# Kernel optimization log

Measured on AMD Instinct MI355X. Metric: run time of the kernel, lower is better.

## Reference

```python
import jax, jax.numpy as jnp
import numpy as np

SEQ, B, N, H, OUT, K, L = 32, 1024, 19, 128, 1, 2, 2


def setup_inputs() -> dict:
    key = jax.random.key(0)
    ks = jax.random.split(key, 16)
    s = lambda i, shape, scale=1.0: (jax.random.normal(ks[i], shape, jnp.float32) * scale)
    return {
        "inputs": s(0, (SEQ, B, N, OUT)),
        "initial_hidden_state": s(1, (L, B, N * H)),
        "support": s(2, (N, N)) * (1.0 / np.sqrt(N)),
        "W_gate0": s(3, (3 * (OUT + H), 2 * H)) * 0.05,
        "b_gate0": s(4, (2 * H,)) * 0.05,
        "W_cand0": s(5, (3 * (OUT + H), H)) * 0.05,
        "b_cand0": s(6, (H,)) * 0.05,
        "W_gate1": s(7, (3 * (H + H), 2 * H)) * 0.05,
        "b_gate1": s(8, (2 * H,)) * 0.05,
        "W_cand1": s(9, (3 * (H + H), H)) * 0.05,
        "b_cand1": s(10, (H,)) * 0.05,
        "W_proj": s(11, (H, OUT)) * 0.05,
        "b_proj": s(12, (OUT,)) * 0.05,
    }


def reference(inputs, initial_hidden_state, support, W_gate0, b_gate0, W_cand0,
              b_cand0, W_gate1, b_gate1, W_cand1, b_cand1, W_proj, b_proj):
    seq_len, batch = inputs.shape[0], inputs.shape[1]
    h0 = initial_hidden_state.reshape(L, batch, N, H)

    def gconv(x, W, b):
        # Chebyshev diffusion: x0, T1=S@x0, T2=2*S@T1-x0 (K=2, 1 support)
        x0 = x
        x1 = jnp.einsum('mn,bnf->bmf', support, x0)
        feats = [x0, x1]
        for _ in range(K - 1):
            x2 = 2.0 * jnp.einsum('mn,bnf->bmf', support, x1) - x0
            feats.append(x2)
            x0, x1 = x1, x2
        X = jnp.concatenate(feats, axis=-1)  # (B, N, F*num_matrices)
        return jnp.einsum('bnf,fo->bno', X, W) + b

    def cell(x_in, h, Wg, bg, Wc, bc):
        ru = jax.nn.sigmoid(gconv(jnp.concatenate([x_in, h], axis=-1), Wg, bg))
        r, u = jnp.split(ru, 2, axis=-1)
        c = jnp.tanh(gconv(jnp.concatenate([x_in, r * h], axis=-1), Wc, bc))
        return u * h + (1.0 - u) * c

    layer_params = [(W_gate0, b_gate0, W_cand0, b_cand0),
                    (W_gate1, b_gate1, W_cand1, b_cand1)]

    def step(carry, _):
        h, cur = carry
        new_h = []
        x = cur
        for i, (Wg, bg, Wc, bc) in enumerate(layer_params):
            x = cell(x, h[i], Wg, bg, Wc, bc)
            new_h.append(x)
        proj = jnp.einsum('bnh,ho->bno', x, W_proj) + b_proj  # (B, N, OUT)
        out_t = proj.reshape(batch, N * OUT)
        return (jnp.stack(new_h, axis=0), proj), out_t

    go = jnp.zeros((batch, N, OUT), inputs.dtype)
    (_, _), outputs = jax.lax.scan(step, (h0, go), None, length=seq_len)
    return outputs  # (seq_len, batch, N*OUT)
```

## Files before the change

### kernel.cpp

```cpp
#include <hip/hip_runtime.h>
#include <hip/hip_bf16.h>
#include <math.h>

#define SEQ   32
#define BATCH 1024
#define NN    19
#define HH    128
#define NB    4
#define MR    (NB*NN)
#define SAS   264
#define H0S   128
#define H1S   132
#define UBS   128
#define NBLK  (BATCH/NB)
#define NT    512
#define UST_S 40

#define OFF_G0 0
#define OFF_C0 122880
#define OFF_G1 184320
#define OFF_C1 380928
#define WTOT   479232

#define OFF_H0  0
#define OFF_H1  19456
#define OFF_SA  59584
#define OFF_UB  101824
#define OFF_SBF 121280
#define OFF_UST 139712
#define OFF_XP  160192
#define LDS_BYTES 160496

__device__ unsigned short g_wall[WTOT];
__device__ unsigned short g_sbf[2*9*512];

typedef __attribute__((ext_vector_type(8))) short  bf16x8;
typedef __attribute__((ext_vector_type(4))) short  bf16x4;
typedef __attribute__((ext_vector_type(4))) float  f32x4;

__device__ __forceinline__ unsigned short f2bf(float v) {
    __hip_bfloat16 b = __float2bfloat16(v);
    return *reinterpret_cast<unsigned short*>(&b);
}
__device__ __forceinline__ float bf2f(unsigned short u) {
    unsigned int x = ((unsigned int)u) << 16;
    return __uint_as_float(x);
}
__device__ __forceinline__ float hload(const unsigned short* p) { return bf2f(*p); }
__device__ __forceinline__ float hload(const float* p)          { return *p; }
__device__ __forceinline__ void  hstore(unsigned short* p, float v) { *p = f2bf(v); }
__device__ __forceinline__ void  hstore(float* p, float v)          { *p = v; }

__global__ __launch_bounds__(256) void wconv_kernel(
    const float* __restrict__ W, int F, int O, int KP, int off, int l0)
{
    int idx = blockIdx.x*256 + threadIdx.x;
    int total = 3*O*KP;
    if (idx >= total) return;
    int j   = idx / (O*KP);
    int r   = idx - j*(O*KP);
    int col = r / KP;
    int k   = r - col*KP;
    int src;
    if (l0) src = (k < HH) ? k+1 : ((k == HH) ? 0 : -1);
    else    src = (k < F) ? k : -1;
    float v = (src >= 0) ? W[(size_t)(j*F + src)*O + col] : 0.f;
    g_wall[off + idx] = f2bf(v);
}

__global__ __launch_bounds__(256) void sbf_kernel(const float* __restrict__ S)
{
    __shared__ float sS[NN*NN], sS2[NN*NN];
    int tid = threadIdx.x;
    for (int i = tid; i < NN*NN; i += 256) sS[i] = S[i];
    __syncthreads();
    for (int i = tid; i < NN*NN; i += 256) {
        int m = i/NN, n = i - m*NN;
        float a = 0.f;
        for (int k = 0; k < NN; ++k) a += sS[m*NN+k]*sS[k*NN+n];
        sS2[i] = a;
    }
    __syncthreads();
    const int fmt[9] = {0,1,2, 1,2,3,4, 3,4};
    const int fkt[9] = {0,0,0, 1,1,1,1, 2,2};
    for (int idx = tid; idx < 2*9*512; idx += 256) {
        int mat = idx / 4608;
        int rem = idx - mat*4608;
        int i   = rem >> 9;
        int l   = (rem >> 3) & 63;
        int e   = rem & 7;
        int r   = fmt[i]*16 + (l & 15);
        int k   = fkt[i]*32 + (l >> 4)*8 + e;
        float v = 0.f;
        if (r < MR) {
            int b = r / NN, m = r - b*NN;
            int k0 = b*NN;
            if (k >= k0 && k < k0 + NN) {
                int n = k - k0;
                v = (mat == 0) ? sS[m*NN+n]
                               : (2.f*sS2[m*NN+n] - ((m==n)?1.f:0.f));
            }
        }
        g_sbf[idx] = f2bf(v);
    }
}

template<int KS, int NTC, bool GATE, int XW, typename HT, int HSTR>
__device__ __forceinline__ void gconv_phase(
    const unsigned short* __restrict__ BT, const float* __restrict__ bias,
    HT* __restrict__ hL,
    unsigned short* __restrict__ sA, unsigned short* __restrict__ ub,
    const unsigned short* __restrict__ sbf, unsigned short* __restrict__ Ust,
    int lane, int w)
{
    constexpr int OC = NTC*128;
    constexpr int KP = KS*32;
    const int r16 = lane & 15, quad = lane >> 4;
    const int sgo = w*(NTC*16);

    const unsigned short* wb[3][NTC];
    #pragma unroll
    for (int j = 0; j < 3; ++j)
        #pragma unroll
        for (int nt = 0; nt < NTC; ++nt)
            wb[j][nt] = BT + (size_t)(j*OC + sgo + nt*16 + r16)*KP + quad*8;

    f32x4 acc[3][5][NTC];
    #pragma unroll
    for (int j = 0; j < 3; ++j)
        #pragma unroll
        for (int mt = 0; mt < 5; ++mt)
            #pragma unroll
            for (int nt = 0; nt < NTC; ++nt) acc[j][mt][nt] = (f32x4)0.f;

    bf16x8 ring[2][3][NTC];
    #pragma unroll
    for (int j = 0; j < 3; ++j)
        #pragma unroll
        for (int nt = 0; nt < NTC; ++nt) {
            ring[0][j][nt] = *(const bf16x8*)(wb[j][nt]);
            if (KS > 1) ring[1][j][nt] = *(const bf16x8*)(wb[j][nt] + 32);
        }
    #pragma unroll
    for (int ks = 0; ks < KS; ++ks) {
        bf16x8 bcur[3][NTC];
        #pragma unroll
        for (int j = 0; j < 3; ++j)
            #pragma unroll
            for (int nt = 0; nt < NTC; ++nt) bcur[j][nt] = ring[ks & 1][j][nt];
        if (ks + 2 < KS) {
            #pragma unroll
            for (int j = 0; j < 3; ++j)
                #pragma unroll
                for (int nt = 0; nt < NTC; ++nt)
                    ring[ks & 1][j][nt] =
                        *(const bf16x8*)(wb[j][nt] + (ks + 2)*32);
        }
        #pragma unroll
        for (int mt = 0; mt < 5; ++mt) {
            bf16x8 af = *(const bf16x8*)&sA[(mt*16 + r16)*SAS + ks*32 + quad*8];
            #pragma unroll
            for (int j = 0; j < 3; ++j)
                #pragma unroll
                for (int nt = 0; nt < NTC; ++nt)
                    acc[j][mt][nt] = __builtin_amdgcn_mfma_f32_16x16x32_bf16(
                        af, bcur[j][nt], acc[j][mt][nt], 0, 0, 0);
        }
    }

    constexpr int ktCnt[3]   = {3,4,2};
    constexpr int ktMT[3][4] = {{0,1,2,0},{1,2,3,4},{3,4,0,0}};
    constexpr int ktF0[3]    = {0,3,7};
    #pragma unroll
    for (int j = 1; j <= 2; ++j) {
        #pragma unroll
        for (int kt = 0; kt < 3; ++kt) {
            if (kt == 2) {
                int zc = lane & 31, zh = lane >> 5;
                *(bf16x8*)&Ust[zc*UST_S + 16 + zh*8] = (bf16x8)(short)0;
            }
            #pragma unroll
            for (int mtk = 0; mtk < 2; ++mtk) {
                constexpr int dummy = 0; (void)dummy;
                int mt = kt*2 + mtk;
                if (kt*2 + mtk < 5) {
                    #pragma unroll
                    for (int nt = 0; nt < NTC; ++nt) {
                        bf16x4 pv;
                        pv[0] = (short)f2bf(acc[j][kt*2+mtk][nt][0]);
                        pv[1] = (short)f2bf(acc[j][kt*2+mtk][nt][1]);
                        pv[2] = (short)f2bf(acc[j][kt*2+mtk][nt][2]);
                        pv[3] = (short)f2bf(acc[j][kt*2+mtk][nt][3]);
                        *(bf16x4*)&Ust[(nt*16 + r16)*UST_S + mtk*16 + quad*4] = pv;
                    }
                }
                (void)mt;
            }
            bf16x8 Bf[NTC];
            #pragma unroll
            for (int nt = 0; nt < NTC; ++nt)
                Bf[nt] = *(const bf16x8*)&Ust[(nt*16 + r16)*UST_S + quad*8];
            #pragma unroll
            for (int q = 0; q < ktCnt[kt]; ++q) {
                const int mt = ktMT[kt][q];
                bf16x8 af = *(const bf16x8*)
                    &sbf[((j-1)*9 + ktF0[kt] + q)*512 + lane*8];
                #pragma unroll
                for (int nt = 0; nt < NTC; ++nt)
                    acc[0][mt][nt] = __builtin_amdgcn_mfma_f32_16x16x32_bf16(
                        af, Bf[nt], acc[0][mt][nt], 0, 0, 0);
            }
        }
    }

    float bv[NTC];
    #pragma unroll
    for (int nt = 0; nt < NTC; ++nt) bv[nt] = bias[sgo + nt*16 + r16];

    if (GATE) __syncthreads();

    #pragma unroll
    for (int mt = 0; mt < 5; ++mt)
        #pragma unroll
        for (int reg = 0; reg < 4; ++reg) {
            int gm = mt*16 + quad*4 + reg;
            if (gm < MR) {
                #pragma unroll
                for (int nt = 0; nt < NTC; ++nt) {
                    int o = sgo + nt*16 + r16;
                    float v = acc[0][mt][nt][reg] + bv[nt];
                    if (GATE) {
                        float sg_ = 1.f/(1.f + __expf(-v));
                        if (o < HH)
                            sA[gm*SAS + XW + o] =
                                f2bf(sg_ * hload(&hL[gm*HSTR + o]));
                        else
                            ub[gm*UBS + (o - HH)] = f2bf(sg_);
                    } else {
                        float c  = 2.f/(1.f + __expf(-2.f*v)) - 1.f;
                        float u  = bf2f(ub[gm*UBS + o]);
                        float ho = hload(&hL[gm*HSTR + o]);
                        hstore(&hL[gm*HSTR + o], u*ho + (1.f - u)*c);
                    }
                }
            }
        }
}

__global__ __launch_bounds__(NT, 2) void dcgru_persistent(
    const float* __restrict__ ihs,
    const float* __restrict__ bg0, const float* __restrict__ bc0,
    const float* __restrict__ bg1, const float* __restrict__ bc1,
    const float* __restrict__ Wp, const float* __restrict__ bp,
    float* __restrict__ out)
{
    extern __shared__ char smem[];
    unsigned short* h0  = (unsigned short*)(smem + OFF_H0);
    float*          h1  = (float*)(smem + OFF_H1);
    unsigned short* sA  = (unsigned short*)(smem + OFF_SA);
    unsigned short* ub  = (unsigned short*)(smem + OFF_UB);
    unsigned short* sbf = (unsigned short*)(smem + OFF_SBF);
    float*       xprev  = (float*)(smem + OFF_XP);

    const int tid  = threadIdx.x;
    const int lane = tid & 63;
    const int w    = tid >> 6;
    const int bb   = blockIdx.x * NB;
    unsigned short* Ust = (unsigned short*)(smem + OFF_UST) + w*(32*UST_S);

    const unsigned short* BTg0 = g_wall + OFF_G0;
    const unsigned short* BTc0 = g_wall + OFF_C0;
    const unsigned short* BTg1 = g_wall + OFF_G1;
    const unsigned short* BTc1 = g_wall + OFF_C1;

    for (int i = tid; i < MR*HH; i += NT) {
        h0[i] = f2bf(ihs[(size_t)bb*2432 + i]);
        h1[(i >> 7)*H1S + (i & 127)] = ihs[(size_t)(BATCH + bb)*2432 + i];
    }
    for (int i = tid; i < MR; i += NT) xprev[i] = 0.f;
    for (int i = tid; i < 80*SAS/8; i += NT) ((bf16x8*)sA)[i] = (bf16x8)(short)0;
    for (int i = tid; i < 2*9*512/8; i += NT)
        ((bf16x8*)sbf)[i] = ((const bf16x8*)g_sbf)[i];
    const float wp0 = Wp[lane], wp1 = Wp[64 + lane], bpv = bp[0];
    __syncthreads();

    for (int t = 0; t < SEQ; ++t) {
        for (int i = tid; i < MR*16; i += NT) {
            int row = i >> 4, ch = i & 15;
            *(bf16x8*)&sA[row*SAS + ch*8] =
                *(const bf16x8*)&h0[row*H0S + ch*8];
        }
        for (int i = tid; i < MR*4; i += NT) {
            int row = i >> 2, ch = i & 3;
            bf16x8 v = (bf16x8)(short)0;
            if (ch == 0) v[0] = (short)f2bf(xprev[row]);
            *(bf16x8*)&sA[row*SAS + HH + ch*8] = v;
        }
        __syncthreads();
        gconv_phase<5,2,true ,0,unsigned short,H0S>(BTg0, bg0, h0, sA, ub, sbf, Ust, lane, w);
        __syncthreads();
        gconv_phase<5,1,false,0,unsigned short,H0S>(BTc0, bc0, h0, sA, ub, sbf, Ust, lane, w);
        __syncthreads();

        for (int i = tid; i < MR*16; i += NT) {
            int row = i >> 4, ch = i & 15;
            *(bf16x8*)&sA[row*SAS + ch*8] =
                *(const bf16x8*)&h0[row*H0S + ch*8];
        }
        for (int i = tid; i < MR*16; i += NT) {
            int row = i >> 4, ch = i & 15;
            const float* hp = &h1[row*H1S + ch*8];
            f32x4 x0 = *(const f32x4*)hp;
            f32x4 x1 = *(const f32x4*)(hp + 4);
            bf16x8 v;
            v[0] = (short)f2bf(x0[0]); v[1] = (short)f2bf(x0[1]);
            v[2] = (short)f2bf(x0[2]); v[3] = (short)f2bf(x0[3]);
            v[4] = (short)f2bf(x1[0]); v[5] = (short)f2bf(x1[1]);
            v[6] = (short)f2bf(x1[2]); v[7] = (short)f2bf(x1[3]);
            *(bf16x8*)&sA[row*SAS + HH + ch*8] = v;
        }
        __syncthreads();
        gconv_phase<8,2,true ,HH,float,H1S>(BTg1, bg1, h1, sA, ub, sbf, Ust, lane, w);
        __syncthreads();
        gconv_phase<8,1,false,HH,float,H1S>(BTc1, bc1, h1, sA, ub, sbf, Ust, lane, w);
        __syncthreads();

        {
            int b  = w >> 1;
            int n0 = (w & 1) ? 10 : 0;
            int n1 = (w & 1) ? 19 : 10;
            for (int n = n0; n < n1; ++n) {
                int row = b*NN + n;
                float s = h1[row*H1S + lane]*wp0 + h1[row*H1S + 64 + lane]*wp1;
                #pragma unroll
                for (int off = 32; off; off >>= 1) s += __shfl_down(s, off, 64);
                if (lane == 0) {
                    float v = s + bpv;
                    out[((size_t)t*BATCH + bb + b)*NN + n] = v;
                    xprev[row] = v;
                }
            }
        }
        __syncthreads();
    }
}

extern "C" void kernel_launch(void* const* d_in, const int* in_sizes, int n_in,
                              void* d_out, int out_size, void* d_ws, size_t ws_size,
                              hipStream_t stream) {
    const float* ihs = (const float*)d_in[1];
    const float* S   = (const float*)d_in[2];
    const float* Wg0 = (const float*)d_in[3];
    const float* bg0 = (const float*)d_in[4];
    const float* Wc0 = (const float*)d_in[5];
    const float* bc0 = (const float*)d_in[6];
    const float* Wg1 = (const float*)d_in[7];
    const float* bg1 = (const float*)d_in[8];
    const float* Wc1 = (const float*)d_in[9];
    const float* bc1 = (const float*)d_in[10];
    const float* Wp  = (const float*)d_in[11];
    const float* bp  = (const float*)d_in[12];
    float* out = (float*)d_out;

    sbf_kernel<<<1, 256, 0, stream>>>(S);
    wconv_kernel<<<(3*256*160+255)/256, 256, 0, stream>>>(Wg0, 129, 256, 160, OFF_G0, 1);
    wconv_kernel<<<(3*128*160+255)/256, 256, 0, stream>>>(Wc0, 129, 128, 160, OFF_C0, 1);
    wconv_kernel<<<(3*256*256+255)/256, 256, 0, stream>>>(Wg1, 256, 256, 256, OFF_G1, 0);
    wconv_kernel<<<(3*128*256+255)/256, 256, 0, stream>>>(Wc1, 256, 128, 256, OFF_C1, 0);

    hipFuncSetAttribute((const void*)dcgru_persistent,
                        hipFuncAttributeMaxDynamicSharedMemorySize, LDS_BYTES);

    dcgru_persistent<<<NBLK, NT, LDS_BYTES, stream>>>(
        ihs, bg0, bc0, bg1, bc1, Wp, bp, out);
}
```

Measured before the change: 2.610 ms.

## Split fused three-way weight GEMM into sequential per-matrix K-loops to cut register pressure

Instead of accumulating all three weight-slice GEMMs (x0, and the two diffusion terms) at once with acc[3][5][NTC], the kernel now runs one K-loop per weight slice. It immediately folds the diffusion slices into the main accumulator through the support MFMAs, then finishes with the identity-term K-loop accumulating in place. This cuts the live accumulator and weight-ring registers to roughly a third, which can lower spills or raise occupancy. In exchange, the A tile in LDS is re-read three times instead of once, and there is less ILP per K step.

After: 4.278 ms. +63.9%, slower.

```diff
diff --git a/kernel.cpp b/kernel.cpp
--- a/kernel.cpp
+++ b/kernel.cpp
@@ -105,6 +105,50 @@
     }
 }
 
+template<int KS, int NTC, bool ACCIN>
+__device__ __forceinline__ void kloop(f32x4 (&acc)[5][NTC],
+    const unsigned short* __restrict__ Wj,
+    const unsigned short* __restrict__ sA,
+    int r16, int quad, int sgo)
+{
+    constexpr int KP = KS*32;
+    const unsigned short* wp[NTC];
+    #pragma unroll
+    for (int nt = 0; nt < NTC; ++nt)
+        wp[nt] = Wj + (size_t)(sgo + nt*16 + r16)*KP + quad*8;
+    if (!ACCIN) {
+        #pragma unroll
+        for (int mt = 0; mt < 5; ++mt)
+            #pragma unroll
+            for (int nt = 0; nt < NTC; ++nt) acc[mt][nt] = (f32x4)0.f;
+    }
+    bf16x8 ring[2][NTC];
+    #pragma unroll
+    for (int nt = 0; nt < NTC; ++nt) {
+        ring[0][nt] = *(const bf16x8*)(wp[nt]);
+        if (KS > 1) ring[1][nt] = *(const bf16x8*)(wp[nt] + 32);
+    }
+    #pragma unroll
+    for (int ks = 0; ks < KS; ++ks) {
+        bf16x8 cur[NTC];
+        #pragma unroll
+        for (int nt = 0; nt < NTC; ++nt) cur[nt] = ring[ks & 1][nt];
+        if (ks + 2 < KS) {
+            #pragma unroll
+            for (int nt = 0; nt < NTC; ++nt)
+                ring[ks & 1][nt] = *(const bf16x8*)(wp[nt] + (ks + 2)*32);
+        }
+        #pragma unroll
+        for (int mt = 0; mt < 5; ++mt) {
+            bf16x8 af = *(const bf16x8*)&sA[(mt*16 + r16)*SAS + ks*32 + quad*8];
+            #pragma unroll
+            for (int nt = 0; nt < NTC; ++nt)
+                acc[mt][nt] = __builtin_amdgcn_mfma_f32_16x16x32_bf16(
+                    af, cur[nt], acc[mt][nt], 0, 0, 0);
+        }
+    }
+}
+
 template<int KS, int NTC, bool GATE, int XW, typename HT, int HSTR>
 __device__ __forceinline__ void gconv_phase(
     const unsigned short* __restrict__ BT, const float* __restrict__ bias,
@@ -118,61 +162,21 @@
     const int r16 = lane & 15, quad = lane >> 4;
     const int sgo = w*(NTC*16);
 
-    const unsigned short* wb[3][NTC];
-    #pragma unroll
-    for (int j = 0; j < 3; ++j)
-        #pragma unroll
-        for (int nt = 0; nt < NTC; ++nt)
-            wb[j][nt] = BT + (size_t)(j*OC + sgo + nt*16 + r16)*KP + quad*8;
-
-    f32x4 acc[3][5][NTC];
-    #pragma unroll
-    for (int j = 0; j < 3; ++j)
-        #pragma unroll
-        for (int mt = 0; mt < 5; ++mt)
-            #pragma unroll
-            for (int nt = 0; nt < NTC; ++nt) acc[j][mt][nt] = (f32x4)0.f;
-
-    bf16x8 ring[2][3][NTC];
-    #pragma unroll
-    for (int j = 0; j < 3; ++j)
-        #pragma unroll
-        for (int nt = 0; nt < NTC; ++nt) {
-            ring[0][j][nt] = *(const bf16x8*)(wb[j][nt]);
-            if (KS > 1) ring[1][j][nt] = *(const bf16x8*)(wb[j][nt] + 32);
-        }
-    #pragma unroll
-    for (int ks = 0; ks < KS; ++ks) {
-        bf16x8 bcur[3][NTC];
-        #pragma unroll
-        for (int j = 0; j < 3; ++j)
-            #pragma unroll
-            for (int nt = 0; nt < NTC; ++nt) bcur[j][nt] = ring[ks & 1][j][nt];
-        if (ks + 2 < KS) {
-            #pragma unroll
-            for (int j = 0; j < 3; ++j)
-                #pragma unroll
-                for (int nt = 0; nt < NTC; ++nt)
-                    ring[ks & 1][j][nt] =
-                        *(const bf16x8*)(wb[j][nt] + (ks + 2)*32);
-        }
-        #pragma unroll
-        for (int mt = 0; mt < 5; ++mt) {
-            bf16x8 af = *(const bf16x8*)&sA[(mt*16 + r16)*SAS + ks*32 + quad*8];
-            #pragma unroll
-            for (int j = 0; j < 3; ++j)
-                #pragma unroll
-                for (int nt = 0; nt < NTC; ++nt)
-                    acc[j][mt][nt] = __builtin_amdgcn_mfma_f32_16x16x32_bf16(
-                        af, bcur[j][nt], acc[j][mt][nt], 0, 0, 0);
-        }
-    }
-
     constexpr int ktCnt[3]   = {3,4,2};
     constexpr int ktMT[3][4] = {{0,1,2,0},{1,2,3,4},{3,4,0,0}};
     constexpr int ktF0[3]    = {0,3,7};
-    #pragma unroll
-    for (int j = 1; j <= 2; ++j) {
+
+    f32x4 acc0[5][NTC];
+    #pragma unroll
+    for (int mt = 0; mt < 5; ++mt)
+        #pragma unroll
+        for (int nt = 0; nt < NTC; ++nt) acc0[mt][nt] = (f32x4)0.f;
+
+    #pragma unroll
+    for (int jj = 1; jj <= 2; ++jj) {
+        f32x4 accT[5][NTC];
+        kloop<KS,NTC,false>(accT, BT + (size_t)jj*OC*KP, sA, r16, quad, sgo);
+
         #pragma unroll
         for (int kt = 0; kt < 3; ++kt) {
             if (kt == 2) {
@@ -181,20 +185,17 @@
             }
             #pragma unroll
             for (int mtk = 0; mtk < 2; ++mtk) {
-                constexpr int dummy = 0; (void)dummy;
-                int mt = kt*2 + mtk;
                 if (kt*2 + mtk < 5) {
                     #pragma unroll
                     for (int nt = 0; nt < NTC; ++nt) {
                         bf16x4 pv;
-                        pv[0] = (short)f2bf(acc[j][kt*2+mtk][nt][0]);
-                        pv[1] = (short)f2bf(acc[j][kt*2+mtk][nt][1]);
-                        pv[2] = (short)f2bf(acc[j][kt*2+mtk][nt][2]);
-                        pv[3] = (short)f2bf(acc[j][kt*2+mtk][nt][3]);
+                        pv[0] = (short)f2bf(accT[kt*2+mtk][nt][0]);
+                        pv[1] = (short)f2bf(accT[kt*2+mtk][nt][1]);
+                        pv[2] = (short)f2bf(accT[kt*2+mtk][nt][2]);
+                        pv[3] = (short)f2bf(accT[kt*2+mtk][nt][3]);
                         *(bf16x4*)&Ust[(nt*16 + r16)*UST_S + mtk*16 + quad*4] = pv;
                     }
                 }
-                (void)mt;
             }
             bf16x8 Bf[NTC];
             #pragma unroll
@@ -204,14 +205,16 @@
             for (int q = 0; q < ktCnt[kt]; ++q) {
                 const int mt = ktMT[kt][q];
                 bf16x8 af = *(const bf16x8*)
-                    &sbf[((j-1)*9 + ktF0[kt] + q)*512 + lane*8];
+                    &sbf[((jj-1)*9 + ktF0[kt] + q)*512 + lane*8];
                 #pragma unroll
                 for (int nt = 0; nt < NTC; ++nt)
-                    acc[0][mt][nt] = __builtin_amdgcn_mfma_f32_16x16x32_bf16(
-                        af, Bf[nt], acc[0][mt][nt], 0, 0, 0);
-            }
-        }
-    }
+                    acc0[mt][nt] = __builtin_amdgcn_mfma_f32_16x16x32_bf16(
+                        af, Bf[nt], acc0[mt][nt], 0, 0, 0);
+            }
+        }
+    }
+
+    kloop<KS,NTC,true>(acc0, BT, sA, r16, quad, sgo);
 
     float bv[NTC];
     #pragma unroll
@@ -228,7 +231,7 @@
                 #pragma unroll
                 for (int nt = 0; nt < NTC; ++nt) {
                     int o = sgo + nt*16 + r16;
-                    float v = acc[0][mt][nt][reg] + bv[nt];
+                    float v = acc0[mt][nt][reg] + bv[nt];
                     if (GATE) {
                         float sg_ = 1.f/(1.f + __expf(-v));
                         if (o < HH)
```

## Double block threads to 1024 and give each wave one 16-column output tile

Applied to the files above, without the earlier changes.

Raises the block size from 512 to 1024 threads so each wave computes a single 16-column output tile instead of NTC tiles. In candidate phases only half of the waves are active. The per-wave Ust staging buffer shrinks, is zero-initialised once, and the projection work is split across 16 waves. This aims to expose more waves for latency hiding and lower per-thread register pressure, at the cost of idle waves in the 128-column phases and more barrier participants. Launch bounds now ask for 4 blocks per SM, but the LDS size is unchanged, so that occupancy may not be reachable.

After: 2.393 ms. 1.09x faster.

```diff
diff --git a/kernel.cpp b/kernel.cpp
--- a/kernel.cpp
+++ b/kernel.cpp
@@ -13,7 +13,7 @@
 #define H1S   132
 #define UBS   128
 #define NBLK  (BATCH/NB)
-#define NT    512
+#define NT    1024
 #define UST_S 40
 
 #define OFF_G0 0
@@ -105,7 +105,7 @@
     }
 }
 
-template<int KS, int NTC, bool GATE, int XW, typename HT, int HSTR>
+template<int KS, int OC, bool GATE, int XW, typename HT, int HSTR>
 __device__ __forceinline__ void gconv_phase(
     const unsigned short* __restrict__ BT, const float* __restrict__ bias,
     HT* __restrict__ hL,
@@ -113,122 +113,94 @@
     const unsigned short* __restrict__ sbf, unsigned short* __restrict__ Ust,
     int lane, int w)
 {
-    constexpr int OC = NTC*128;
     constexpr int KP = KS*32;
     const int r16 = lane & 15, quad = lane >> 4;
-    const int sgo = w*(NTC*16);
-
-    const unsigned short* wb[3][NTC];
-    #pragma unroll
-    for (int j = 0; j < 3; ++j)
-        #pragma unroll
-        for (int nt = 0; nt < NTC; ++nt)
-            wb[j][nt] = BT + (size_t)(j*OC + sgo + nt*16 + r16)*KP + quad*8;
-
-    f32x4 acc[3][5][NTC];
-    #pragma unroll
-    for (int j = 0; j < 3; ++j)
-        #pragma unroll
-        for (int mt = 0; mt < 5; ++mt)
-            #pragma unroll
-            for (int nt = 0; nt < NTC; ++nt) acc[j][mt][nt] = (f32x4)0.f;
-
-    bf16x8 ring[2][3][NTC];
-    #pragma unroll
-    for (int j = 0; j < 3; ++j)
-        #pragma unroll
-        for (int nt = 0; nt < NTC; ++nt) {
-            ring[0][j][nt] = *(const bf16x8*)(wb[j][nt]);
-            if (KS > 1) ring[1][j][nt] = *(const bf16x8*)(wb[j][nt] + 32);
-        }
-    #pragma unroll
-    for (int ks = 0; ks < KS; ++ks) {
-        bf16x8 bcur[3][NTC];
-        #pragma unroll
-        for (int j = 0; j < 3; ++j)
-            #pragma unroll
-            for (int nt = 0; nt < NTC; ++nt) bcur[j][nt] = ring[ks & 1][j][nt];
-        if (ks + 2 < KS) {
-            #pragma unroll
-            for (int j = 0; j < 3; ++j)
-                #pragma unroll
-                for (int nt = 0; nt < NTC; ++nt)
-                    ring[ks & 1][j][nt] =
-                        *(const bf16x8*)(wb[j][nt] + (ks + 2)*32);
-        }
-        #pragma unroll
-        for (int mt = 0; mt < 5; ++mt) {
-            bf16x8 af = *(const bf16x8*)&sA[(mt*16 + r16)*SAS + ks*32 + quad*8];
-            #pragma unroll
-            for (int j = 0; j < 3; ++j)
-                #pragma unroll
-                for (int nt = 0; nt < NTC; ++nt)
-                    acc[j][mt][nt] = __builtin_amdgcn_mfma_f32_16x16x32_bf16(
-                        af, bcur[j][nt], acc[j][mt][nt], 0, 0, 0);
-        }
-    }
+    const int sgo = w*16;
+    const bool act = (sgo < OC);
 
     constexpr int ktCnt[3]   = {3,4,2};
     constexpr int ktMT[3][4] = {{0,1,2,0},{1,2,3,4},{3,4,0,0}};
     constexpr int ktF0[3]    = {0,3,7};
-    #pragma unroll
-    for (int j = 1; j <= 2; ++j) {
-        #pragma unroll
-        for (int kt = 0; kt < 3; ++kt) {
-            if (kt == 2) {
-                int zc = lane & 31, zh = lane >> 5;
-                *(bf16x8*)&Ust[zc*UST_S + 16 + zh*8] = (bf16x8)(short)0;
-            }
-            #pragma unroll
-            for (int mtk = 0; mtk < 2; ++mtk) {
-                constexpr int dummy = 0; (void)dummy;
-                int mt = kt*2 + mtk;
-                if (kt*2 + mtk < 5) {
-                    #pragma unroll
-                    for (int nt = 0; nt < NTC; ++nt) {
+
+    f32x4 acc[3][5];
+    if (act) {
+        const unsigned short* wb[3];
+        #pragma unroll
+        for (int j = 0; j < 3; ++j)
+            wb[j] = BT + (size_t)(j*OC + sgo + r16)*KP + quad*8;
+
+        #pragma unroll
+        for (int j = 0; j < 3; ++j)
+            #pragma unroll
+            for (int mt = 0; mt < 5; ++mt) acc[j][mt] = (f32x4)0.f;
+
+        bf16x8 ring[2][3];
+        #pragma unroll
+        for (int j = 0; j < 3; ++j) {
+            ring[0][j] = *(const bf16x8*)(wb[j]);
+            if (KS > 1) ring[1][j] = *(const bf16x8*)(wb[j] + 32);
+        }
+        #pragma unroll
+        for (int ks = 0; ks < KS; ++ks) {
+            bf16x8 bcur[3];
+            #pragma unroll
+            for (int j = 0; j < 3; ++j) bcur[j] = ring[ks & 1][j];
+            if (ks + 2 < KS) {
+                #pragma unroll
+                for (int j = 0; j < 3; ++j)
+                    ring[ks & 1][j] = *(const bf16x8*)(wb[j] + (ks + 2)*32);
+            }
+            #pragma unroll
+            for (int mt = 0; mt < 5; ++mt) {
+                bf16x8 af = *(const bf16x8*)&sA[(mt*16 + r16)*SAS + ks*32 + quad*8];
+                #pragma unroll
+                for (int j = 0; j < 3; ++j)
+                    acc[j][mt] = __builtin_amdgcn_mfma_f32_16x16x32_bf16(
+                        af, bcur[j], acc[j][mt], 0, 0, 0);
+            }
+        }
+
+        #pragma unroll
+        for (int jj = 1; jj <= 2; ++jj) {
+            #pragma unroll
+            for (int kt = 0; kt < 3; ++kt) {
+                #pragma unroll
+                for (int mtk = 0; mtk < 2; ++mtk) {
+                    if (kt*2 + mtk < 5) {
                         bf16x4 pv;
-                        pv[0] = (short)f2bf(acc[j][kt*2+mtk][nt][0]);
-                        pv[1] = (short)f2bf(acc[j][kt*2+mtk][nt][1]);
-                        pv[2] = (short)f2bf(acc[j][kt*2+mtk][nt][2]);
-                        pv[3] = (short)f2bf(acc[j][kt*2+mtk][nt][3]);
-                        *(bf16x4*)&Ust[(nt*16 + r16)*UST_S + mtk*16 + quad*4] = pv;
+                        pv[0] = (short)f2bf(acc[jj][kt*2+mtk][0]);
+                        pv[1] = (short)f2bf(acc[jj][kt*2+mtk][1]);
+                        pv[2] = (short)f2bf(acc[jj][kt*2+mtk][2]);
+                        pv[3] = (short)f2bf(acc[jj][kt*2+mtk][3]);
+                        *(bf16x4*)&Ust[r16*UST_S + mtk*16 + quad*4] = pv;
                     }
                 }
-                (void)mt;
-            }
-            bf16x8 Bf[NTC];
-            #pragma unroll
-            for (int nt = 0; nt < NTC; ++nt)
-                Bf[nt] = *(const bf16x8*)&Ust[(nt*16 + r16)*UST_S + quad*8];
-            #pragma unroll
-            for (int q = 0; q < ktCnt[kt]; ++q) {
-                const int mt = ktMT[kt][q];
-                bf16x8 af = *(const bf16x8*)
-                    &sbf[((j-1)*9 + ktF0[kt] + q)*512 + lane*8];
-                #pragma unroll
-                for (int nt = 0; nt < NTC; ++nt)
-                    acc[0][mt][nt] = __builtin_amdgcn_mfma_f32_16x16x32_bf16(
-                        af, Bf[nt], acc[0][mt][nt], 0, 0, 0);
-            }
-        }
-    }
-
-    float bv[NTC];
-    #pragma unroll
-    for (int nt = 0; nt < NTC; ++nt) bv[nt] = bias[sgo + nt*16 + r16];
+                bf16x8 Bf = *(const bf16x8*)&Ust[r16*UST_S + quad*8];
+                #pragma unroll
+                for (int q = 0; q < ktCnt[kt]; ++q) {
+                    const int mt = ktMT[kt][q];
+                    bf16x8 af = *(const bf16x8*)
+                        &sbf[((jj-1)*9 + ktF0[kt] + q)*512 + lane*8];
+                    acc[0][mt] = __builtin_amdgcn_mfma_f32_16x16x32_bf16(
+                        af, Bf, acc[0][mt], 0, 0, 0);
+                }
+            }
+        }
+    }
+
+    float bv = act ? bias[sgo + r16] : 0.f;
 
     if (GATE) __syncthreads();
 
-    #pragma unroll
-    for (int mt = 0; mt < 5; ++mt)
-        #pragma unroll
-        for (int reg = 0; reg < 4; ++reg) {
-            int gm = mt*16 + quad*4 + reg;
-            if (gm < MR) {
-                #pragma unroll
-                for (int nt = 0; nt < NTC; ++nt) {
-                    int o = sgo + nt*16 + r16;
-                    float v = acc[0][mt][nt][reg] + bv[nt];
+    if (act) {
+        #pragma unroll
+        for (int mt = 0; mt < 5; ++mt)
+            #pragma unroll
+            for (int reg = 0; reg < 4; ++reg) {
+                int gm = mt*16 + quad*4 + reg;
+                if (gm < MR) {
+                    int o = sgo + r16;
+                    float v = acc[0][mt][reg] + bv;
                     if (GATE) {
                         float sg_ = 1.f/(1.f + __expf(-v));
                         if (o < HH)
@@ -244,10 +216,10 @@
                     }
                 }
             }
-        }
-}
-
-__global__ __launch_bounds__(NT, 2) void dcgru_persistent(
+    }
+}
+
+__global__ __launch_bounds__(NT, 4) void dcgru_persistent(
     const float* __restrict__ ihs,
     const float* __restrict__ bg0, const float* __restrict__ bc0,
     const float* __restrict__ bg1, const float* __restrict__ bc1,
@@ -266,7 +238,7 @@
     const int lane = tid & 63;
     const int w    = tid >> 6;
     const int bb   = blockIdx.x * NB;
-    unsigned short* Ust = (unsigned short*)(smem + OFF_UST) + w*(32*UST_S);
+    unsigned short* Ust = (unsigned short*)(smem + OFF_UST) + w*(16*UST_S);
 
     const unsigned short* BTg0 = g_wall + OFF_G0;
     const unsigned short* BTc0 = g_wall + OFF_C0;
@@ -279,6 +251,8 @@
     }
     for (int i = tid; i < MR; i += NT) xprev[i] = 0.f;
     for (int i = tid; i < 80*SAS/8; i += NT) ((bf16x8*)sA)[i] = (bf16x8)(short)0;
+    for (int i = tid; i < 16*16*UST_S/8; i += NT)
+        ((bf16x8*)(smem + OFF_UST))[i] = (bf16x8)(short)0;
     for (int i = tid; i < 2*9*512/8; i += NT)
         ((bf16x8*)sbf)[i] = ((const bf16x8*)g_sbf)[i];
     const float wp0 = Wp[lane], wp1 = Wp[64 + lane], bpv = bp[0];
@@ -297,9 +271,9 @@
             *(bf16x8*)&sA[row*SAS + HH + ch*8] = v;
         }
         __syncthreads();
-        gconv_phase<5,2,true ,0,unsigned short,H0S>(BTg0, bg0, h0, sA, ub, sbf, Ust, lane, w);
-        __syncthreads();
-        gconv_phase<5,1,false,0,unsigned short,H0S>(BTc0, bc0, h0, sA, ub, sbf, Ust, lane, w);
+        gconv_phase<5,256,true ,0,unsigned short,H0S>(BTg0, bg0, h0, sA, ub, sbf, Ust, lane, w);
+        __syncthreads();
+        gconv_phase<5,128,false,0,unsigned short,H0S>(BTc0, bc0, h0, sA, ub, sbf, Ust, lane, w);
         __syncthreads();
 
         for (int i = tid; i < MR*16; i += NT) {
@@ -320,15 +294,15 @@
             *(bf16x8*)&sA[row*SAS + HH + ch*8] = v;
         }
         __syncthreads();
-        gconv_phase<8,2,true ,HH,float,H1S>(BTg1, bg1, h1, sA, ub, sbf, Ust, lane, w);
-        __syncthreads();
-        gconv_phase<8,1,false,HH,float,H1S>(BTc1, bc1, h1, sA, ub, sbf, Ust, lane, w);
+        gconv_phase<8,256,true ,HH,float,H1S>(BTg1, bg1, h1, sA, ub, sbf, Ust, lane, w);
+        __syncthreads();
+        gconv_phase<8,128,false,HH,float,H1S>(BTc1, bc1, h1, sA, ub, sbf, Ust, lane, w);
         __syncthreads();
 
         {
-            int b  = w >> 1;
-            int n0 = (w & 1) ? 10 : 0;
-            int n1 = (w & 1) ? 19 : 10;
+            int b  = w >> 2;
+            int n0 = (w & 3) * 5;
+            int n1 = n0 + 5; if (n1 > NN) n1 = NN;
             for (int n = n0; n < n1; ++n) {
                 int row = b*NN + n;
                 float s = h1[row*H1S + lane]*wp0 + h1[row*H1S + 64 + lane]*wp1;
```
